# Optimization experiments

Hardware: AMD Instinct MI355X
Metric: run time of the kernel (lower is better)

## Reference

```python
import jax, jax.numpy as jnp
import numpy as np

N_NODES = 100000


def gcn_layer(x, row, col, ew, W, b, n_nodes):
    # PyG GCNConv: add self-loops (weight 1), symmetric normalization
    # deg^{-1/2}[row] * w * deg^{-1/2}[col], linear transform, scatter-add to col.
    loop = jnp.arange(n_nodes, dtype=row.dtype)
    row_f = jnp.concatenate([row, loop])
    col_f = jnp.concatenate([col, loop])
    ew_f = jnp.concatenate([ew, jnp.ones((n_nodes,), dtype=ew.dtype)])
    deg = jax.ops.segment_sum(ew_f, col_f, num_segments=n_nodes)  # [N]
    dinv = jnp.where(deg > 0, jax.lax.rsqrt(deg), 0.0)
    norm = dinv[row_f] * ew_f * dinv[col_f]  # [E+N]
    h = x @ W  # [N, F_out]
    msg = norm[:, None] * h[row_f]  # [E+N, F_out]
    out = jax.ops.segment_sum(msg, col_f, num_segments=n_nodes)
    return out + b


def setup_inputs() -> dict:
    key = jax.random.key(0)
    ks = jax.random.split(key, 6)
    n, e, d_in, d_h = N_NODES, 3200000, 128, 16
    x = jax.random.normal(ks[0], (n, d_in), dtype=jnp.float32)
    edge_index = jax.random.randint(ks[1], (2, e), 0, n, dtype=jnp.int64)
    edge_weight = jax.random.uniform(ks[2], (e,), dtype=jnp.float32)
    W1 = jax.random.normal(ks[3], (d_in, d_h), dtype=jnp.float32) * (1.0 / np.sqrt(d_in))
    b1 = jnp.zeros((d_h,), dtype=jnp.float32)
    W2 = jax.random.normal(ks[4], (d_h, 1), dtype=jnp.float32) * (1.0 / np.sqrt(d_h))
    b2 = jnp.zeros((1,), dtype=jnp.float32)
    return {"x": x, "edge_index": edge_index, "edge_weight": edge_weight,
            "W1": W1, "b1": b1, "W2": W2, "b2": b2}


def reference(x, edge_index, edge_weight, W1, b1, W2, b2):
    row, col = edge_index[0], edge_index[1]
    n = x.shape[0]
    h = gcn_layer(x, row, col, edge_weight, W1, b1, n)
    h = jax.nn.relu(h)
    out = gcn_layer(h, row, col, edge_weight, W2, b2, n)
    return out.squeeze(-1)  # [N]
```

## Files before the change

### kernel.cpp

```cpp
#include <hip/hip_runtime.h>


#define DH 16
#define BSH 7
#define BNODES 128
#define NB_MAX 784
#define CHUNK 4096

__global__ __launch_bounds__(256) void k_Ahist(const int* __restrict__ col,
                                               int* __restrict__ gCnt, int E, int NB) {
    __shared__ int lh[NB_MAX];
    const int tid = threadIdx.x;
    for (int i = tid; i < NB; i += 256) lh[i] = 0;
    __syncthreads();
    const int base = blockIdx.x * CHUNK;
    #pragma unroll
    for (int k = 0; k < 16; ++k) {
        int e = base + tid + 256 * k;
        if (e < E) atomicAdd(&lh[col[e] >> BSH], 1);
    }
    __syncthreads();
    for (int i = tid; i < NB; i += 256) {
        int v = lh[i];
        if (v) atomicAdd(&gCnt[i], v);
    }
}

__global__ __launch_bounds__(1024) void k_Ascan(const int* __restrict__ gCnt,
                                                int* __restrict__ gBase,
                                                int* __restrict__ gCursor,
                                                int NB, int E) {
    __shared__ int s[1024];
    const int t = threadIdx.x;
    int v = (t < NB) ? gCnt[t] : 0;
    s[t] = v;
    __syncthreads();
    for (int off = 1; off < 1024; off <<= 1) {
        int u = (t >= off) ? s[t - off] : 0;
        __syncthreads();
        s[t] += u;
        __syncthreads();
    }
    if (t < NB) {
        int ex = s[t] - v;
        gBase[t] = ex;
        gCursor[t] = ex;
    }
    if (t == 0) gBase[NB] = E;
}

__global__ __launch_bounds__(256) void k_Ascatter(const int* __restrict__ row,
                                                  const int* __restrict__ col,
                                                  const float* __restrict__ ew,
                                                  int* __restrict__ gCursor,
                                                  uint2* __restrict__ edata,
                                                  int E, int NB) {
    __shared__ int lh[NB_MAX], lbase[NB_MAX], lcur[NB_MAX];
    const int tid = threadIdx.x;
    for (int i = tid; i < NB; i += 256) lh[i] = 0;
    __syncthreads();
    const int base = blockIdx.x * CHUNK;
    int r_[16], c_[16];
    float w_[16];
    #pragma unroll
    for (int k = 0; k < 16; ++k) {
        int e = base + tid + 256 * k;
        bool ok = e < E;
        c_[k] = ok ? col[e] : -1;
        r_[k] = ok ? row[e] : 0;
        w_[k] = ok ? ew[e] : 0.f;
        if (ok) atomicAdd(&lh[c_[k] >> BSH], 1);
    }
    __syncthreads();
    for (int b = tid; b < NB; b += 256) {
        int v = lh[b];
        if (v) {
            lbase[b] = atomicAdd(&gCursor[b], v);
            lcur[b] = 0;
        }
    }
    __syncthreads();
    #pragma unroll
    for (int k = 0; k < 16; ++k) {
        if (c_[k] >= 0) {
            int b = c_[k] >> BSH;
            int rem = c_[k] & (BNODES - 1);
            int off = atomicAdd(&lcur[b], 1);
            edata[lbase[b] + off] =
                make_uint2((unsigned)r_[k] | ((unsigned)rem << 20), __float_as_uint(w_[k]));
        }
    }
}

__global__ __launch_bounds__(256) void k_deg(const int* __restrict__ gBase,
                                             const uint2* __restrict__ edata,
                                             float* __restrict__ dinv, int N) {
    __shared__ float dg[BNODES];
    const int tid = threadIdx.x;
    if (tid < BNODES) dg[tid] = 0.f;
    __syncthreads();
    const int s = gBase[blockIdx.x], e = gBase[blockIdx.x + 1];
    for (int i = s + tid; i < e; i += 256) {
        uint2 ed = edata[i];
        atomicAdd(&dg[ed.x >> 20], __uint_as_float(ed.y));
    }
    __syncthreads();
    int node = (blockIdx.x << BSH) + tid;
    if (tid < BNODES && node < N) dinv[node] = rsqrtf(dg[tid] + 1.0f);
}

__global__ __launch_bounds__(256) void k_h1(const float* __restrict__ x,
                                            const float* __restrict__ W1,
                                            float* __restrict__ h) {
    __shared__ float Ws[128 * DH];
    __shared__ float xs[16 * 132];
    const int t = threadIdx.x;
    const int node0 = blockIdx.x * 16;
    #pragma unroll
    for (int i = 0; i < 8; ++i) Ws[t + 256 * i] = W1[t + 256 * i];
    const float4* xg = (const float4*)(x + (size_t)node0 * 128);
    #pragma unroll
    for (int it = 0; it < 2; ++it) {
        int idx = t + 256 * it;
        int n = idx >> 5, k4 = idx & 31;
        float4 v = xg[n * 32 + k4];
        *(float4*)(&xs[n * 132 + k4 * 4]) = v;
    }
    __syncthreads();
    const int node = t >> 4, feat = t & 15;
    const float* xr = &xs[node * 132];
    float acc = 0.f;
    #pragma unroll 8
    for (int k = 0; k < 128; ++k) acc += xr[k] * Ws[k * DH + feat];
    h[(size_t)(node0 + node) * DH + feat] = acc;
}

__global__ __launch_bounds__(256) void k_gather1(
    const int* __restrict__ gBase, const uint2* __restrict__ edata,
    const float* __restrict__ dinv, const float* __restrict__ h,
    const float* __restrict__ b1, const float* __restrict__ W2,
    float* __restrict__ q, int N) {
    __shared__ float acc[DH][BNODES + 1];
    __shared__ float b1s[DH], W2s[DH];
    const int tid = threadIdx.x;
    if (tid < DH) { b1s[tid] = b1[tid]; W2s[tid] = W2[tid]; }
    for (int i = tid; i < DH * (BNODES + 1); i += 256) ((float*)acc)[i] = 0.f;
    __syncthreads();
    const int s = gBase[blockIdx.x], e = gBase[blockIdx.x + 1];
    const int g = tid >> 4, f = tid & 15;
    for (int i = s + g; i < e; i += 16) {
        uint2 ed = edata[i];
        int r = ed.x & 0xFFFFF;
        int rem = ed.x >> 20;
        float w = __uint_as_float(ed.y);
        atomicAdd(&acc[f][rem], w * dinv[r] * h[r * DH + f]);
    }
    __syncthreads();
    int node = (blockIdx.x << BSH) + tid;
    if (tid < BNODES && node < N) {
        float dc = dinv[node];
        float t = 0.f;
        #pragma unroll
        for (int ff = 0; ff < DH; ++ff) {
            float ag = dc * acc[ff][tid] + dc * dc * h[node * DH + ff];
            t += fmaxf(ag + b1s[ff], 0.f) * W2s[ff];
        }
        q[node] = dc * t;
    }
}

__global__ __launch_bounds__(256) void k_gather2(
    const int* __restrict__ gBase, const uint2* __restrict__ edata,
    const float* __restrict__ dinv, const float* __restrict__ q,
    const float* __restrict__ b2, float* __restrict__ out, int N) {
    __shared__ float a2[BNODES];
    const int tid = threadIdx.x;
    if (tid < BNODES) a2[tid] = 0.f;
    __syncthreads();
    const int s = gBase[blockIdx.x], e = gBase[blockIdx.x + 1];
    for (int i = s + tid; i < e; i += 256) {
        uint2 ed = edata[i];
        int r = ed.x & 0xFFFFF;
        atomicAdd(&a2[ed.x >> 20], __uint_as_float(ed.y) * q[r]);
    }
    __syncthreads();
    int node = (blockIdx.x << BSH) + tid;
    if (tid < BNODES && node < N)
        out[node] = b2[0] + dinv[node] * (a2[tid] + q[node]);
}

extern "C" void kernel_launch(void* const* d_in, const int* in_sizes, int n_in,
                              void* d_out, int out_size, void* d_ws, size_t ws_size,
                              hipStream_t stream) {
    const float* x  = (const float*)d_in[0];
    const int*   ei = (const int*)d_in[1];
    const float* ew = (const float*)d_in[2];
    const float* W1 = (const float*)d_in[3];
    const float* b1 = (const float*)d_in[4];
    const float* W2 = (const float*)d_in[5];
    const float* b2 = (const float*)d_in[6];
    float* out = (float*)d_out;

    const int N = in_sizes[0] / 128;
    const int E = in_sizes[2];
    const int* row = ei;
    const int* col = ei + E;
    const int NB = (N + BNODES - 1) >> BSH;

    int* gCnt    = (int*)d_ws;
    int* gBase   = gCnt + NB;
    int* gCursor = gBase + NB + 1;
    float* dinv  = (float*)(gCursor + NB);
    float* h     = dinv + N;
    float* q     = h + (size_t)16 * N;
    uintptr_t ep = (uintptr_t)(q + N);
    ep = (ep + 7) & ~(uintptr_t)7;
    uint2* edata = (uint2*)ep;

    const int ablocks = (E + CHUNK - 1) / CHUNK;

    hipMemsetAsync(gCnt, 0, (size_t)NB * sizeof(int), stream);
    k_Ahist<<<ablocks, 256, 0, stream>>>(col, gCnt, E, NB);
    k_Ascan<<<1, 1024, 0, stream>>>(gCnt, gBase, gCursor, NB, E);
    k_Ascatter<<<ablocks, 256, 0, stream>>>(row, col, ew, gCursor, edata, E, NB);
    k_deg<<<NB, 256, 0, stream>>>(gBase, edata, dinv, N);
    k_h1<<<N / 16, 256, 0, stream>>>(x, W1, h);
    k_gather1<<<NB, 256, 0, stream>>>(gBase, edata, dinv, h, b1, W2, q, N);
    k_gather2<<<NB, 256, 0, stream>>>(gBase, edata, dinv, q, b2, out, N);
}
```

Measured before the change: 589.9 us.

## Split layer-1 gather across slices per node block with partial-sum finalize kernel

The layer-1 gather now launches NSLICE blocks per node bucket, each handling an interleaved subset of that bucket's edges and writing per-slice partial accumulators to workspace. A new finalize kernel sums the slices and applies bias, ReLU and the W2 projection. Both gather loops are unrolled by two to keep more independent loads in flight. This raises occupancy, since only about 782 blocks ran before, at the cost of an extra kernel launch and partial-buffer traffic.

```diff
diff --git a/kernel.cpp b/kernel.cpp
--- a/kernel.cpp
+++ b/kernel.cpp
@@ -6,6 +6,7 @@
 #define BNODES 128
 #define NB_MAX 784
 #define CHUNK 4096
+#define NSLICE 4
 
 __global__ __launch_bounds__(256) void k_Ahist(const int* __restrict__ col,
                                                int* __restrict__ gCnt, int E, int NB) {
@@ -138,25 +139,51 @@
 __global__ __launch_bounds__(256) void k_gather1(
     const int* __restrict__ gBase, const uint2* __restrict__ edata,
     const float* __restrict__ dinv, const float* __restrict__ h,
-    const float* __restrict__ b1, const float* __restrict__ W2,
-    float* __restrict__ q, int N) {
+    float* __restrict__ partial) {
+    __shared__ float acc[DH][BNODES + 1];
+    const int tid = threadIdx.x;
+    for (int i = tid; i < DH * (BNODES + 1); i += 256) ((float*)acc)[i] = 0.f;
+    __syncthreads();
+    const int b = blockIdx.x, sl = blockIdx.y;
+    const int s = gBase[b], e = gBase[b + 1];
+    const int g = tid >> 4, f = tid & 15;
+    for (int i = s + sl * 16 + g; i < e; i += 128) {
+        uint2 ed0 = edata[i];
+        int i1 = i + 64;
+        uint2 ed1 = (i1 < e) ? edata[i1] : make_uint2(0u, 0u);
+        int r0 = ed0.x & 0xFFFFF;
+        int r1 = ed1.x & 0xFFFFF;
+        float w0 = __uint_as_float(ed0.y), w1 = __uint_as_float(ed1.y);
+        float v0 = w0 * dinv[r0] * h[r0 * DH + f];
+        float v1 = w1 * dinv[r1] * h[r1 * DH + f];
+        atomicAdd(&acc[f][ed0.x >> 20], v0);
+        atomicAdd(&acc[f][ed1.x >> 20], v1);
+    }
+    __syncthreads();
+    float* ps = partial + ((size_t)b * NSLICE + sl) * (DH * BNODES);
+    #pragma unroll
+    for (int i = tid; i < DH * BNODES; i += 256)
+        ps[i] = acc[i >> BSH][i & (BNODES - 1)];
+}
+
+__global__ __launch_bounds__(256) void k_fin1(
+    const float* __restrict__ partial, const float* __restrict__ dinv,
+    const float* __restrict__ h, const float* __restrict__ b1,
+    const float* __restrict__ W2, float* __restrict__ q, int N) {
     __shared__ float acc[DH][BNODES + 1];
     __shared__ float b1s[DH], W2s[DH];
     const int tid = threadIdx.x;
     if (tid < DH) { b1s[tid] = b1[tid]; W2s[tid] = W2[tid]; }
-    for (int i = tid; i < DH * (BNODES + 1); i += 256) ((float*)acc)[i] = 0.f;
-    __syncthreads();
-    const int s = gBase[blockIdx.x], e = gBase[blockIdx.x + 1];
-    const int g = tid >> 4, f = tid & 15;
-    for (int i = s + g; i < e; i += 16) {
-        uint2 ed = edata[i];
-        int r = ed.x & 0xFFFFF;
-        int rem = ed.x >> 20;
-        float w = __uint_as_float(ed.y);
-        atomicAdd(&acc[f][rem], w * dinv[r] * h[r * DH + f]);
-    }
-    __syncthreads();
-    int node = (blockIdx.x << BSH) + tid;
+    const int b = blockIdx.x;
+    const float* ps = partial + (size_t)b * NSLICE * (DH * BNODES);
+    for (int i = tid; i < DH * BNODES; i += 256) {
+        float s = 0.f;
+        #pragma unroll
+        for (int sl = 0; sl < NSLICE; ++sl) s += ps[sl * (DH * BNODES) + i];
+        acc[i >> BSH][i & (BNODES - 1)] = s;
+    }
+    __syncthreads();
+    int node = (b << BSH) + tid;
     if (tid < BNODES && node < N) {
         float dc = dinv[node];
         float t = 0.f;
@@ -178,10 +205,14 @@
     if (tid < BNODES) a2[tid] = 0.f;
     __syncthreads();
     const int s = gBase[blockIdx.x], e = gBase[blockIdx.x + 1];
-    for (int i = s + tid; i < e; i += 256) {
-        uint2 ed = edata[i];
-        int r = ed.x & 0xFFFFF;
-        atomicAdd(&a2[ed.x >> 20], __uint_as_float(ed.y) * q[r]);
+    for (int i = s + tid; i < e; i += 512) {
+        uint2 ed0 = edata[i];
+        int i1 = i + 256;
+        uint2 ed1 = (i1 < e) ? edata[i1] : make_uint2(0u, 0u);
+        float v0 = __uint_as_float(ed0.y) * q[ed0.x & 0xFFFFF];
+        float v1 = __uint_as_float(ed1.y) * q[ed1.x & 0xFFFFF];
+        atomicAdd(&a2[ed0.x >> 20], v0);
+        atomicAdd(&a2[ed1.x >> 20], v1);
     }
     __syncthreads();
     int node = (blockIdx.x << BSH) + tid;
@@ -213,7 +244,8 @@
     float* dinv  = (float*)(gCursor + NB);
     float* h     = dinv + N;
     float* q     = h + (size_t)16 * N;
-    uintptr_t ep = (uintptr_t)(q + N);
+    float* partial = q + N;
+    uintptr_t ep = (uintptr_t)(partial + (size_t)NB * NSLICE * (DH * BNODES));
     ep = (ep + 7) & ~(uintptr_t)7;
     uint2* edata = (uint2*)ep;
 
@@ -225,6 +257,7 @@
     k_Ascatter<<<ablocks, 256, 0, stream>>>(row, col, ew, gCursor, edata, E, NB);
     k_deg<<<NB, 256, 0, stream>>>(gBase, edata, dinv, N);
     k_h1<<<N / 16, 256, 0, stream>>>(x, W1, h);
-    k_gather1<<<NB, 256, 0, stream>>>(gBase, edata, dinv, h, b1, W2, q, N);
+    k_gather1<<<dim3(NB, NSLICE), 256, 0, stream>>>(gBase, edata, dinv, h, partial);
+    k_fin1<<<NB, 256, 0, stream>>>(partial, dinv, h, b1, W2, q, N);
     k_gather2<<<NB, 256, 0, stream>>>(gBase, edata, dinv, q, b2, out, N);
 }
```

Result: faster. 533.1 us (-9.6%).

## Stage scatter in LDS for coalesced writes, prescale h by dinv, vectorize gathers

Applied to the files above, without the earlier changes.

The bucket scatter now sorts each chunk's edges into a shared-memory staging buffer through a local prefix scan, then writes them to global memory in contiguous order. Previously each edge was written to a scattered address. h is pre-multiplied by dinv in k_h1, which removes the per-edge dinv[r] gather in gather1. gather1 now processes one edge per thread, loading float4 rows with two edges per iteration, and gather2 is unrolled by two. The staging buffers add about 40KB of LDS per block, which may lower occupancy, and a leftover dead loop remains in the scatter kernel.

```diff
diff --git a/kernel.cpp b/kernel.cpp
--- a/kernel.cpp
+++ b/kernel.cpp
@@ -55,7 +55,12 @@
                                                   int* __restrict__ gCursor,
                                                   uint2* __restrict__ edata,
                                                   int E, int NB) {
-    __shared__ int lh[NB_MAX], lbase[NB_MAX], lcur[NB_MAX];
+    __shared__ int lh[NB_MAX];
+    __shared__ int lbase[NB_MAX];
+    __shared__ int lcur[NB_MAX];
+    __shared__ int tsum[256];
+    __shared__ unsigned short sbuck[CHUNK];
+    __shared__ uint2 stage[CHUNK];
     const int tid = threadIdx.x;
     for (int i = tid; i < NB; i += 256) lh[i] = 0;
     __syncthreads();
@@ -72,11 +77,34 @@
         if (ok) atomicAdd(&lh[c_[k] >> BSH], 1);
     }
     __syncthreads();
+    const int t0 = tid * 4;
+    int c0 = (t0 + 0 < NB) ? lh[t0 + 0] : 0;
+    int c1 = (t0 + 1 < NB) ? lh[t0 + 1] : 0;
+    int c2 = (t0 + 2 < NB) ? lh[t0 + 2] : 0;
+    int c3 = (t0 + 3 < NB) ? lh[t0 + 3] : 0;
+    int mysum = c0 + c1 + c2 + c3;
+    tsum[tid] = mysum;
+    __syncthreads();
+    for (int off = 1; off < 256; off <<= 1) {
+        int u = (tid >= off) ? tsum[tid - off] : 0;
+        __syncthreads();
+        tsum[tid] += u;
+        __syncthreads();
+    }
+    int p = tsum[tid] - mysum;
+    if (t0 + 0 < NB) { lbase[t0 + 0] = p; lcur[t0 + 0] = p; } p += c0;
+    if (t0 + 1 < NB) { lbase[t0 + 1] = p; lcur[t0 + 1] = p; } p += c1;
+    if (t0 + 2 < NB) { lbase[t0 + 2] = p; lcur[t0 + 2] = p; } p += c2;
+    if (t0 + 3 < NB) { lbase[t0 + 3] = p; lcur[t0 + 3] = p; } p += c3;
+    __syncthreads();
     for (int b = tid; b < NB; b += 256) {
-        int v = lh[b];
-        if (v) {
-            lbase[b] = atomicAdd(&gCursor[b], v);
-            lcur[b] = 0;
+        int cnt = lcur[b];
+    }
+    for (int b = tid; b < NB; b += 256) {
+        int cnt = lh[b];
+        if (cnt) {
+            int g = atomicAdd(&gCursor[b], cnt);
+            lh[b] = g - lbase[b];
         }
     }
     __syncthreads();
@@ -84,12 +112,17 @@
     for (int k = 0; k < 16; ++k) {
         if (c_[k] >= 0) {
             int b = c_[k] >> BSH;
-            int rem = c_[k] & (BNODES - 1);
-            int off = atomicAdd(&lcur[b], 1);
-            edata[lbase[b] + off] =
-                make_uint2((unsigned)r_[k] | ((unsigned)rem << 20), __float_as_uint(w_[k]));
+            unsigned rem = (unsigned)(c_[k] & (BNODES - 1));
+            int sp = atomicAdd(&lcur[b], 1);
+            stage[sp] = make_uint2((unsigned)r_[k] | (rem << 20), __float_as_uint(w_[k]));
+            sbuck[sp] = (unsigned short)b;
         }
     }
+    __syncthreads();
+    int nE = E - base;
+    if (nE > CHUNK) nE = CHUNK;
+    for (int j = tid; j < nE; j += 256)
+        edata[lh[sbuck[j]] + j] = stage[j];
 }
 
 __global__ __launch_bounds__(256) void k_deg(const int* __restrict__ gBase,
@@ -111,7 +144,8 @@
 
 __global__ __launch_bounds__(256) void k_h1(const float* __restrict__ x,
                                             const float* __restrict__ W1,
-                                            float* __restrict__ h) {
+                                            const float* __restrict__ dinv,
+                                            float* __restrict__ hd) {
     __shared__ float Ws[128 * DH];
     __shared__ float xs[16 * 132];
     const int t = threadIdx.x;
@@ -132,38 +166,67 @@
     float acc = 0.f;
     #pragma unroll 8
     for (int k = 0; k < 128; ++k) acc += xr[k] * Ws[k * DH + feat];
-    h[(size_t)(node0 + node) * DH + feat] = acc;
+    const int v = node0 + node;
+    hd[(size_t)v * DH + feat] = dinv[v] * acc;
 }
 
 __global__ __launch_bounds__(256) void k_gather1(
     const int* __restrict__ gBase, const uint2* __restrict__ edata,
-    const float* __restrict__ dinv, const float* __restrict__ h,
+    const float* __restrict__ hd, const float* __restrict__ dinv,
     const float* __restrict__ b1, const float* __restrict__ W2,
     float* __restrict__ q, int N) {
-    __shared__ float acc[DH][BNODES + 1];
+    __shared__ float acc[BNODES][DH + 1];
     __shared__ float b1s[DH], W2s[DH];
     const int tid = threadIdx.x;
     if (tid < DH) { b1s[tid] = b1[tid]; W2s[tid] = W2[tid]; }
-    for (int i = tid; i < DH * (BNODES + 1); i += 256) ((float*)acc)[i] = 0.f;
-    __syncthreads();
-    const int s = gBase[blockIdx.x], e = gBase[blockIdx.x + 1];
-    const int g = tid >> 4, f = tid & 15;
-    for (int i = s + g; i < e; i += 16) {
-        uint2 ed = edata[i];
-        int r = ed.x & 0xFFFFF;
-        int rem = ed.x >> 20;
-        float w = __uint_as_float(ed.y);
-        atomicAdd(&acc[f][rem], w * dinv[r] * h[r * DH + f]);
-    }
-    __syncthreads();
-    int node = (blockIdx.x << BSH) + tid;
+    for (int i = tid; i < BNODES * (DH + 1); i += 256) ((float*)acc)[i] = 0.f;
+    __syncthreads();
+    const int b = blockIdx.x;
+    const int s = gBase[b], e = gBase[b + 1];
+    for (int i = s + tid; i < e; i += 512) {
+        uint2 ed0 = edata[i];
+        int i1 = i + 256;
+        uint2 ed1 = (i1 < e) ? edata[i1] : make_uint2(0u, 0u);
+        int r0 = ed0.x & 0xFFFFF, rem0 = ed0.x >> 20;
+        int r1 = ed1.x & 0xFFFFF, rem1 = ed1.x >> 20;
+        float w0 = __uint_as_float(ed0.y), w1 = __uint_as_float(ed1.y);
+        const float4* h0 = (const float4*)(hd + (size_t)r0 * DH);
+        const float4* h1 = (const float4*)(hd + (size_t)r1 * DH);
+        float4 A0 = h0[0], B0 = h0[1], C0 = h0[2], D0 = h0[3];
+        float4 A1 = h1[0], B1 = h1[1], C1 = h1[2], D1 = h1[3];
+        float* a0 = acc[rem0];
+        atomicAdd(a0 + 0,  w0 * A0.x); atomicAdd(a0 + 1,  w0 * A0.y);
+        atomicAdd(a0 + 2,  w0 * A0.z); atomicAdd(a0 + 3,  w0 * A0.w);
+        atomicAdd(a0 + 4,  w0 * B0.x); atomicAdd(a0 + 5,  w0 * B0.y);
+        atomicAdd(a0 + 6,  w0 * B0.z); atomicAdd(a0 + 7,  w0 * B0.w);
+        atomicAdd(a0 + 8,  w0 * C0.x); atomicAdd(a0 + 9,  w0 * C0.y);
+        atomicAdd(a0 + 10, w0 * C0.z); atomicAdd(a0 + 11, w0 * C0.w);
+        atomicAdd(a0 + 12, w0 * D0.x); atomicAdd(a0 + 13, w0 * D0.y);
+        atomicAdd(a0 + 14, w0 * D0.z); atomicAdd(a0 + 15, w0 * D0.w);
+        float* a1 = acc[rem1];
+        atomicAdd(a1 + 0,  w1 * A1.x); atomicAdd(a1 + 1,  w1 * A1.y);
+        atomicAdd(a1 + 2,  w1 * A1.z); atomicAdd(a1 + 3,  w1 * A1.w);
+        atomicAdd(a1 + 4,  w1 * B1.x); atomicAdd(a1 + 5,  w1 * B1.y);
+        atomicAdd(a1 + 6,  w1 * B1.z); atomicAdd(a1 + 7,  w1 * B1.w);
+        atomicAdd(a1 + 8,  w1 * C1.x); atomicAdd(a1 + 9,  w1 * C1.y);
+        atomicAdd(a1 + 10, w1 * C1.z); atomicAdd(a1 + 11, w1 * C1.w);
+        atomicAdd(a1 + 12, w1 * D1.x); atomicAdd(a1 + 13, w1 * D1.y);
+        atomicAdd(a1 + 14, w1 * D1.z); atomicAdd(a1 + 15, w1 * D1.w);
+    }
+    __syncthreads();
+    int node = (b << BSH) + tid;
     if (tid < BNODES && node < N) {
         float dc = dinv[node];
+        const float4* hs = (const float4*)(hd + (size_t)node * DH);
         float t = 0.f;
         #pragma unroll
-        for (int ff = 0; ff < DH; ++ff) {
-            float ag = dc * acc[ff][tid] + dc * dc * h[node * DH + ff];
-            t += fmaxf(ag + b1s[ff], 0.f) * W2s[ff];
+        for (int qd = 0; qd < 4; ++qd) {
+            float4 hv = hs[qd];
+            int f = qd * 4;
+            t += fmaxf(dc * (acc[tid][f + 0] + hv.x) + b1s[f + 0], 0.f) * W2s[f + 0];
+            t += fmaxf(dc * (acc[tid][f + 1] + hv.y) + b1s[f + 1], 0.f) * W2s[f + 1];
+            t += fmaxf(dc * (acc[tid][f + 2] + hv.z) + b1s[f + 2], 0.f) * W2s[f + 2];
+            t += fmaxf(dc * (acc[tid][f + 3] + hv.w) + b1s[f + 3], 0.f) * W2s[f + 3];
         }
         q[node] = dc * t;
     }
@@ -178,10 +241,14 @@
     if (tid < BNODES) a2[tid] = 0.f;
     __syncthreads();
     const int s = gBase[blockIdx.x], e = gBase[blockIdx.x + 1];
-    for (int i = s + tid; i < e; i += 256) {
-        uint2 ed = edata[i];
-        int r = ed.x & 0xFFFFF;
-        atomicAdd(&a2[ed.x >> 20], __uint_as_float(ed.y) * q[r]);
+    for (int i = s + tid; i < e; i += 512) {
+        uint2 ed0 = edata[i];
+        int i1 = i + 256;
+        uint2 ed1 = (i1 < e) ? edata[i1] : make_uint2(0u, 0u);
+        float v0 = __uint_as_float(ed0.y) * q[ed0.x & 0xFFFFF];
+        float v1 = __uint_as_float(ed1.y) * q[ed1.x & 0xFFFFF];
+        atomicAdd(&a2[ed0.x >> 20], v0);
+        atomicAdd(&a2[ed1.x >> 20], v1);
     }
     __syncthreads();
     int node = (blockIdx.x << BSH) + tid;
@@ -211,8 +278,8 @@
     int* gBase   = gCnt + NB;
     int* gCursor = gBase + NB + 1;
     float* dinv  = (float*)(gCursor + NB);
-    float* h     = dinv + N;
-    float* q     = h + (size_t)16 * N;
+    float* hd    = dinv + N;
+    float* q     = hd + (size_t)16 * N;
     uintptr_t ep = (uintptr_t)(q + N);
     ep = (ep + 7) & ~(uintptr_t)7;
     uint2* edata = (uint2*)ep;
@@ -224,7 +291,7 @@
     k_Ascan<<<1, 1024, 0, stream>>>(gCnt, gBase, gCursor, NB, E);
     k_Ascatter<<<ablocks, 256, 0, stream>>>(row, col, ew, gCursor, edata, E, NB);
     k_deg<<<NB, 256, 0, stream>>>(gBase, edata, dinv, N);
-    k_h1<<<N / 16, 256, 0, stream>>>(x, W1, h);
-    k_gather1<<<NB, 256, 0, stream>>>(gBase, edata, dinv, h, b1, W2, q, N);
+    k_h1<<<N / 16, 256, 0, stream>>>(x, W1, dinv, hd);
+    k_gather1<<<NB, 256, 0, stream>>>(gBase, edata, hd, dinv, b1, W2, q, N);
     k_gather2<<<NB, 256, 0, stream>>>(gBase, edata, dinv, q, b2, out, N);
 }
```

After: 592.8 us. Within noise of the previous version (+0.5%).
